# Kernel optimization log

Hardware: AMD Instinct MI355X
Metric: run time of the kernel (lower is better)

The kernel has to match this reference:

```python
import jax, jax.numpy as jnp
import numpy as np

EPS = 1e-5

def _layernorm(x, w, b):
    mu = jnp.mean(x, axis=-1, keepdims=True)
    var = jnp.mean(jnp.square(x - mu), axis=-1, keepdims=True)
    return (x - mu) * jax.lax.rsqrt(var + EPS) * w + b

def setup_inputs() -> dict:
    key = jax.random.key(0)
    ks = jax.random.split(key, 8)
    B, N, C, D = 32, 1024, 4096, 64
    x = jax.random.normal(ks[0], (B, N, C), dtype=jnp.float32)
    gumbel = jax.random.gumbel(ks[1], (B, N, 2), dtype=jnp.float32)
    ln_w = jnp.ones((C,), jnp.float32)
    ln_b = jnp.zeros((C,), jnp.float32)
    w1 = jax.random.normal(ks[2], (C, D), dtype=jnp.float32) * 0.02
    b1 = jnp.zeros((D,), jnp.float32)
    w2 = jax.random.normal(ks[3], (D, 2), dtype=jnp.float32) * 0.02
    b2 = jnp.zeros((2,), jnp.float32)
    return {"x": x, "gumbel": gumbel, "ln_w": ln_w, "ln_b": ln_b,
            "w1": w1, "b1": b1, "w2": w2, "b2": b2}

def reference(x, gumbel, ln_w, ln_b, w1, b1, w2, b2):
    B, N, C = x.shape
    xn = _layernorm(x, ln_w, ln_b)
    local_x = xn[:, :, : C // 2]                      # [B, N, C/2]
    # policy is all-ones -> weighted mean over tokens
    global_x = jnp.mean(xn[:, :, C // 2:], axis=1, keepdims=True)  # [B, 1, C/2]
    feat = jnp.concatenate(
        [local_x, jnp.broadcast_to(global_x, local_x.shape)], axis=-1)  # [B, N, C]
    h = jax.nn.gelu(feat @ w1 + b1, approximate=False)  # [B, N, 64]
    logits = h @ w2 + b2                                # [B, N, 2]
    pred_score = jax.nn.log_softmax(logits, axis=-1)
    # gumbel-softmax (tau=1, hard=True) with straight-through estimator
    y_soft = jax.nn.softmax(pred_score + gumbel, axis=-1)
    hard = jax.nn.one_hot(jnp.argmax(y_soft, axis=-1), 2, dtype=y_soft.dtype)
    y = hard - jax.lax.stop_gradient(y_soft) + y_soft
    keep = y[:, :, 0]                                   # [B, N]
    # dense equivalent of masked_select/split: zero out dropped tokens
    return x * keep[:, :, None]
```

## Files before the change

### kernel.cpp

```cpp
#include <hip/hip_runtime.h>
#include <math.h>

#define B_   32
#define N_   1024
#define C_   4096
#define HC_  2048
#define D_   64
#define NT_  32768
#define BKC_ 32
#define NCH_ (HC_ / BKC_)
#define AST_ 68

__device__ __forceinline__ float4 ld4(const float* p) {
    return *reinterpret_cast<const float4*>(p);
}

__global__ __launch_bounds__(256) void mk1(
        const float* __restrict__ x, const float* __restrict__ lnw,
        const float* __restrict__ lnb, const float* __restrict__ w1,
        float* __restrict__ Pp, float* __restrict__ muv,
        float* __restrict__ rsv, float* __restrict__ part) {
    __shared__ float smem[8704];
    __shared__ float sLow[64], qLow[64];

    float* As0 = smem;
    float* As1 = smem + 2176;
    float* Bs0 = smem + 4352;
    float* Bs1 = smem + 6400;

    const int t = threadIdx.x;
    const int tid = blockIdx.x;
    const int T0 = tid * 64;
    const int rt = t & 15;
    const int dt = t >> 4;
    const int row = t >> 2;
    const int fq = t & 3;
    const int lane = t & 63, w = t >> 6;

    float acc[16];
#pragma unroll
    for (int i = 0; i < 16; ++i) acc[i] = 0.f;
    float sR = 0.f, qR = 0.f;

    float4 xv1, xv2, wv1, wv2;
    float lw1, lw2;
    {
        const float* rp = x + (size_t)(T0 + row) * C_;
        xv1 = ld4(rp + fq * 4);
        xv2 = ld4(rp + 16 + fq * 4);
        const float4* s4 = reinterpret_cast<const float4*>(w1);
        wv1 = s4[t]; wv2 = s4[256 + t];
        lw1 = lnw[t >> 4];
        lw2 = lnw[16 + (t >> 4)];
    }

#pragma unroll 1
    for (int c = 0; c < NCH_; ++c) {
        float* Ab = (c & 1) ? As1 : As0;
        float* Bb = (c & 1) ? Bs1 : Bs0;
        {
            const int kb1 = fq * 4, kb2 = 16 + fq * 4;
            Ab[(kb1 + 0) * AST_ + row] = xv1.x;
            Ab[(kb1 + 1) * AST_ + row] = xv1.y;
            Ab[(kb1 + 2) * AST_ + row] = xv1.z;
            Ab[(kb1 + 3) * AST_ + row] = xv1.w;
            Ab[(kb2 + 0) * AST_ + row] = xv2.x;
            Ab[(kb2 + 1) * AST_ + row] = xv2.y;
            Ab[(kb2 + 2) * AST_ + row] = xv2.z;
            Ab[(kb2 + 3) * AST_ + row] = xv2.w;
            sR += ((xv1.x + xv1.y) + (xv1.z + xv1.w))
                + ((xv2.x + xv2.y) + (xv2.z + xv2.w));
            qR = fmaf(xv1.x, xv1.x, fmaf(xv1.y, xv1.y,
                 fmaf(xv1.z, xv1.z, fmaf(xv1.w, xv1.w, qR))));
            qR = fmaf(xv2.x, xv2.x, fmaf(xv2.y, xv2.y,
                 fmaf(xv2.z, xv2.z, fmaf(xv2.w, xv2.w, qR))));
        }
        {
            float4 v1 = wv1, v2 = wv2;
            v1.x *= lw1; v1.y *= lw1; v1.z *= lw1; v1.w *= lw1;
            v2.x *= lw2; v2.y *= lw2; v2.z *= lw2; v2.w *= lw2;
            float4* b4 = reinterpret_cast<float4*>(Bb);
            b4[t] = v1;
            b4[256 + t] = v2;
        }
        __syncthreads();
        if (c + 1 < NCH_) {
            const int k1 = (c + 1) * BKC_;
            const float* rp = x + (size_t)(T0 + row) * C_ + k1;
            xv1 = ld4(rp + fq * 4);
            xv2 = ld4(rp + 16 + fq * 4);
            const float4* s4 = reinterpret_cast<const float4*>(
                w1 + (size_t)k1 * D_);
            wv1 = s4[t]; wv2 = s4[256 + t];
            lw1 = lnw[k1 + (t >> 4)];
            lw2 = lnw[k1 + 16 + (t >> 4)];
        }
#pragma unroll
        for (int k = 0; k < BKC_; ++k) {
            const float4 a4 = *reinterpret_cast<const float4*>(
                Ab + k * AST_ + rt * 4);
            const float4 b4 = *reinterpret_cast<const float4*>(
                Bb + k * 64 + dt * 4);
            const float av[4] = {a4.x, a4.y, a4.z, a4.w};
            const float bv[4] = {b4.x, b4.y, b4.z, b4.w};
#pragma unroll
            for (int ri = 0; ri < 4; ++ri)
#pragma unroll
                for (int cj = 0; cj < 4; ++cj)
                    acc[ri * 4 + cj] =
                        fmaf(av[ri], bv[cj], acc[ri * 4 + cj]);
        }
    }
#pragma unroll
    for (int ri = 0; ri < 4; ++ri) {
        float* dst = Pp + (size_t)(T0 + rt * 4 + ri) * D_ + dt * 4;
        *reinterpret_cast<float4*>(dst) = make_float4(
            acc[ri * 4 + 0], acc[ri * 4 + 1],
            acc[ri * 4 + 2], acc[ri * 4 + 3]);
    }
    sR += __shfl_xor(sR, 1); qR += __shfl_xor(qR, 1);
    sR += __shfl_xor(sR, 2); qR += __shfl_xor(qR, 2);
    if (fq == 0) { sLow[row] = sR; qLow[row] = qR; }
    __syncthreads();

    float4 wv[8], bv[8], gacc[8];
#pragma unroll
    for (int m = 0; m < 8; ++m) {
        wv[m] = ld4(lnw + HC_ + (m * 64 + lane) * 4);
        bv[m] = ld4(lnb + HC_ + (m * 64 + lane) * 4);
        gacc[m] = make_float4(0.f, 0.f, 0.f, 0.f);
    }
    for (int i = 0; i < 16; ++i) {
        const int r = w * 16 + i;
        const int tok = T0 + r;
        const float* rowp = x + (size_t)tok * C_ + HC_;
        float4 v[8];
        float s = 0.f, q = 0.f;
#pragma unroll
        for (int m = 0; m < 8; ++m) {
            v[m] = ld4(rowp + (m * 64 + lane) * 4);
            s += (v[m].x + v[m].y) + (v[m].z + v[m].w);
            q = fmaf(v[m].x, v[m].x, fmaf(v[m].y, v[m].y,
                fmaf(v[m].z, v[m].z, fmaf(v[m].w, v[m].w, q))));
        }
#pragma unroll
        for (int o = 1; o < 64; o <<= 1) {
            s += __shfl_xor(s, o);
            q += __shfl_xor(q, o);
        }
        const float S = s + sLow[r];
        const float Q = q + qLow[r];
        const float mu = S * (1.f / C_);
        const float rs = rsqrtf(Q * (1.f / C_) - mu * mu + 1e-5f);
        if (lane == 0) {
            muv[tok] = mu;
            rsv[tok] = rs;
        }
#pragma unroll
        for (int m = 0; m < 8; ++m) {
            gacc[m].x += (v[m].x - mu) * rs * wv[m].x + bv[m].x;
            gacc[m].y += (v[m].y - mu) * rs * wv[m].y + bv[m].y;
            gacc[m].z += (v[m].z - mu) * rs * wv[m].z + bv[m].z;
            gacc[m].w += (v[m].w - mu) * rs * wv[m].w + bv[m].w;
        }
    }
    float (*sh)[HC_] = reinterpret_cast<float(*)[HC_]>(smem);
#pragma unroll
    for (int m = 0; m < 8; ++m)
        *reinterpret_cast<float4*>(&sh[w][(m * 64 + lane) * 4]) = gacc[m];
    __syncthreads();
    float* pp = part + (size_t)tid * HC_;
#pragma unroll
    for (int m = 0; m < 8; ++m) {
        const int j = (m * 64 + lane) * 4;
        const float4 a0 = ld4(&sh[0][j]);
        const float4 a1 = ld4(&sh[1][j]);
        const float4 a2 = ld4(&sh[2][j]);
        const float4 a3 = ld4(&sh[3][j]);
        float4 r;
        r.x = (a0.x + a1.x) + (a2.x + a3.x);
        r.y = (a0.y + a1.y) + (a2.y + a3.y);
        r.z = (a0.z + a1.z) + (a2.z + a3.z);
        r.w = (a0.w + a1.w) + (a2.w + a3.w);
        if (w == (m & 3))
            *reinterpret_cast<float4*>(pp + j) = r;
    }
}

__global__ __launch_bounds__(256) void k2a_part(
        const float* __restrict__ part, const float* __restrict__ w1,
        const float* __restrict__ lnw, const float* __restrict__ lnb,
        float* __restrict__ gpart, float* __restrict__ Wpart,
        float* __restrict__ Bpart) {
    __shared__ float Gs[256];
    __shared__ float red[512];
    const int t = threadIdx.x;
    const int d = t & 63, s = t >> 6;
    const int blk = blockIdx.x;
    if (blk < 256) {
        const int b = blk >> 3, jq = blk & 7;
        const int j = jq * 256 + t;
        float a = 0.f;
        for (int k = 0; k < 16; ++k)
            a += part[(size_t)(b * 16 + k) * HC_ + j];
        Gs[t] = a;
        __syncthreads();
        float acc = 0.f;
        const int j0 = jq * 256 + s * 64;
        for (int jj = 0; jj < 64; ++jj)
            acc = fmaf(Gs[s * 64 + jj],
                       w1[(size_t)(HC_ + j0 + jj) * D_ + d], acc);
        red[s * 64 + d] = acc;
        __syncthreads();
        if (s == 0)
            gpart[(size_t)blk * 64 + d] =
                red[d] + red[64 + d] + red[128 + d] + red[192 + d];
    } else {
        const int wq = blk - 256;
        const int c0 = wq * 256 + s * 64;
        float a = 0.f, c2 = 0.f;
        for (int c = c0; c < c0 + 64; ++c) {
            const float wvv = w1[(size_t)c * D_ + d];
            a = fmaf(lnw[c], wvv, a);
            c2 = fmaf(lnb[c], wvv, c2);
        }
        red[s * 64 + d] = a;
        red[256 + s * 64 + d] = c2;
        __syncthreads();
        if (s == 0) {
            Wpart[wq * 64 + d] =
                red[d] + red[64 + d] + red[128 + d] + red[192 + d];
            Bpart[wq * 64 + d] = red[256 + d] + red[320 + d]
                               + red[384 + d] + red[448 + d];
        }
    }
}

__global__ __launch_bounds__(256) void k45_decide_mask(
        const float* __restrict__ Pp, const float* __restrict__ muv,
        const float* __restrict__ rsv, const float* __restrict__ gpart,
        const float* __restrict__ Wpart, const float* __restrict__ Bpart,
        const float* __restrict__ b1, const float* __restrict__ w2,
        const float* __restrict__ b2, const float* __restrict__ gum,
        const float* __restrict__ x, float* __restrict__ out) {
    const int t = threadIdx.x;
    const int lane = t & 63, w = t >> 6;
    const int token = blockIdx.x * 4 + w;
    const int b = token >> 10;

    float W1 = 0.f, Bsv = 0.f, gt = 0.f;
#pragma unroll
    for (int q = 0; q < 8; ++q) {
        W1 += Wpart[q * 64 + lane];
        Bsv += Bpart[q * 64 + lane];
        gt += gpart[(size_t)(b * 8 + q) * 64 + lane];
    }
    gt *= (1.f / N_);

    const float2 gv = *reinterpret_cast<const float2*>(gum + token * 2);
    const float p = Pp[(size_t)token * D_ + lane];
    const float mu = muv[token], rs = rsv[token];
    float h = rs * (p - mu * W1) + Bsv + gt + b1[lane];
    h = 0.5f * h * (1.f + erff(h * 0.70710678118654752f));
    const float2 w2v = *reinterpret_cast<const float2*>(w2 + lane * 2);
    float l0 = h * w2v.x;
    float l1 = h * w2v.y;
#pragma unroll
    for (int o = 1; o < 64; o <<= 1) {
        l0 += __shfl_xor(l0, o);
        l1 += __shfl_xor(l1, o);
    }
    const float z0 = l0 + b2[0] + gv.x;
    const float z1 = l1 + b2[1] + gv.y;

    float4* dst = reinterpret_cast<float4*>(out + (size_t)token * C_);
    if (z0 >= z1) {
        const float4* src =
            reinterpret_cast<const float4*>(x + (size_t)token * C_);
#pragma unroll
        for (int c = 0; c < 16; ++c)
            dst[c * 64 + lane] = src[c * 64 + lane];
    } else {
        const float4 z = make_float4(0.f, 0.f, 0.f, 0.f);
#pragma unroll
        for (int c = 0; c < 16; ++c)
            dst[c * 64 + lane] = z;
    }
}

extern "C" void kernel_launch(void* const* d_in, const int* in_sizes, int n_in,
                              void* d_out, int out_size, void* d_ws,
                              size_t ws_size, hipStream_t stream) {
    const float* x   = (const float*)d_in[0];
    const float* gum = (const float*)d_in[1];
    const float* lnw = (const float*)d_in[2];
    const float* lnb = (const float*)d_in[3];
    const float* w1  = (const float*)d_in[4];
    const float* b1  = (const float*)d_in[5];
    const float* w2  = (const float*)d_in[6];
    const float* b2  = (const float*)d_in[7];
    float* out = (float*)d_out;

    float* wsf   = (float*)d_ws;
    float* Pp    = wsf;
    float* muv   = Pp + (size_t)NT_ * D_;
    float* rsv   = muv + NT_;
    float* part  = rsv + NT_;
    float* gpart = part + (size_t)512 * HC_;
    float* Wpart = gpart + 256 * 64;
    float* Bpart = Wpart + 8 * 64;

    mk1<<<512, 256, 0, stream>>>(x, lnw, lnb, w1, Pp, muv, rsv, part);
    k2a_part<<<264, 256, 0, stream>>>(part, w1, lnw, lnb,
                                      gpart, Wpart, Bpart);
    k45_decide_mask<<<NT_ / 4, 256, 0, stream>>>(Pp, muv, rsv, gpart,
                                                 Wpart, Bpart, b1, w2, b2,
                                                 gum, x, out);
}
```

Baseline: 370.8 us.

## Use split-bf16 MFMA for local projection with fp32 cleanup for near-tie tokens

Replaces the fp32 FMA tile GEMM in the first kernel with bf16 MFMA using a hi/lo split of both activations and pre-scaled weights (three MFMAs per tile) to approximate fp32 accuracy. A prep kernel packs lnw*w1 into bf16 hi/lo fragments. Tokens whose logit margin falls within a small tolerance are recomputed in fp32 by a new cleanup kernel, which rewrites their output row if the keep decision flips. This adds two launches and some extra traffic in exchange for moving the main GEMM onto matrix cores.

```diff
diff --git a/kernel.cpp b/kernel.cpp
--- a/kernel.cpp
+++ b/kernel.cpp
@@ -9,115 +9,137 @@
 #define NT_  32768
 #define BKC_ 32
 #define NCH_ (HC_ / BKC_)
-#define AST_ 68
+#define TAU_ 0.01f
+
+typedef __attribute__((ext_vector_type(8))) short s16x8;
+typedef __attribute__((ext_vector_type(4))) float f32x4;
 
 __device__ __forceinline__ float4 ld4(const float* p) {
     return *reinterpret_cast<const float4*>(p);
 }
-
-__global__ __launch_bounds__(256) void mk1(
+__device__ __forceinline__ unsigned short f2bf(float f) {
+    unsigned int u = __float_as_uint(f);
+    u += 0x7fffu + ((u >> 16) & 1u);
+    return (unsigned short)(u >> 16);
+}
+__device__ __forceinline__ float bf2f(unsigned short s) {
+    return __uint_as_float(((unsigned int)s) << 16);
+}
+
+__global__ __launch_bounds__(64) void k0_prep(
+        const float* __restrict__ lnw, const float* __restrict__ w1,
+        short* __restrict__ whG, short* __restrict__ wlG) {
+    const int lane = threadIdx.x;
+    const int c = blockIdx.x >> 2, ct = blockIdx.x & 3;
+    s16x8 hv, lv;
+#pragma unroll
+    for (int j = 0; j < 8; ++j) {
+        const int k = c * 32 + (lane >> 4) * 8 + j;
+        const int col = ct * 16 + (lane & 15);
+        const float v = lnw[k] * w1[(size_t)k * D_ + col];
+        const unsigned short h = f2bf(v);
+        hv[j] = (short)h;
+        lv[j] = (short)f2bf(v - bf2f(h));
+    }
+    const size_t base = ((size_t)(c * 4 + ct) * 64 + lane) * 8;
+    *reinterpret_cast<s16x8*>(whG + base) = hv;
+    *reinterpret_cast<s16x8*>(wlG + base) = lv;
+}
+
+__global__ __launch_bounds__(256) void mk1m(
         const float* __restrict__ x, const float* __restrict__ lnw,
-        const float* __restrict__ lnb, const float* __restrict__ w1,
-        float* __restrict__ Pp, float* __restrict__ muv,
-        float* __restrict__ rsv, float* __restrict__ part) {
-    __shared__ float smem[8704];
+        const float* __restrict__ lnb, const short* __restrict__ whG,
+        const short* __restrict__ wlG, float* __restrict__ Pp,
+        float* __restrict__ muv, float* __restrict__ rsv,
+        float* __restrict__ part) {
+    __shared__ float smem[8192];
     __shared__ float sLow[64], qLow[64];
-
-    float* As0 = smem;
-    float* As1 = smem + 2176;
-    float* Bs0 = smem + 4352;
-    float* Bs1 = smem + 6400;
+    short* S = reinterpret_cast<short*>(smem);
 
     const int t = threadIdx.x;
     const int tid = blockIdx.x;
     const int T0 = tid * 64;
-    const int rt = t & 15;
-    const int dt = t >> 4;
-    const int row = t >> 2;
-    const int fq = t & 3;
+    const int row = t >> 2, fq = t & 3;
     const int lane = t & 63, w = t >> 6;
 
-    float acc[16];
-#pragma unroll
-    for (int i = 0; i < 16; ++i) acc[i] = 0.f;
+    f32x4 acc[4];
+#pragma unroll
+    for (int ct = 0; ct < 4; ++ct)
+#pragma unroll
+        for (int r = 0; r < 4; ++r) acc[ct][r] = 0.f;
     float sR = 0.f, qR = 0.f;
 
-    float4 xv1, xv2, wv1, wv2;
-    float lw1, lw2;
+    float4 xv1, xv2;
+    s16x8 bh[4], bl[4], bh2[4], bl2[4];
     {
         const float* rp = x + (size_t)(T0 + row) * C_;
-        xv1 = ld4(rp + fq * 4);
-        xv2 = ld4(rp + 16 + fq * 4);
-        const float4* s4 = reinterpret_cast<const float4*>(w1);
-        wv1 = s4[t]; wv2 = s4[256 + t];
-        lw1 = lnw[t >> 4];
-        lw2 = lnw[16 + (t >> 4)];
+        xv1 = ld4(rp + fq * 8);
+        xv2 = ld4(rp + fq * 8 + 4);
+        const s16x8* wp = reinterpret_cast<const s16x8*>(whG);
+        const s16x8* lp = reinterpret_cast<const s16x8*>(wlG);
+#pragma unroll
+        for (int ct = 0; ct < 4; ++ct) {
+            bh[ct] = wp[(size_t)ct * 64 + lane];
+            bl[ct] = lp[(size_t)ct * 64 + lane];
+        }
     }
 
 #pragma unroll 1
     for (int c = 0; c < NCH_; ++c) {
-        float* Ab = (c & 1) ? As1 : As0;
-        float* Bb = (c & 1) ? Bs1 : Bs0;
+        short* H = S + (c & 1) * 4096;
+        short* L = H + 2048;
         {
-            const int kb1 = fq * 4, kb2 = 16 + fq * 4;
-            Ab[(kb1 + 0) * AST_ + row] = xv1.x;
-            Ab[(kb1 + 1) * AST_ + row] = xv1.y;
-            Ab[(kb1 + 2) * AST_ + row] = xv1.z;
-            Ab[(kb1 + 3) * AST_ + row] = xv1.w;
-            Ab[(kb2 + 0) * AST_ + row] = xv2.x;
-            Ab[(kb2 + 1) * AST_ + row] = xv2.y;
-            Ab[(kb2 + 2) * AST_ + row] = xv2.z;
-            Ab[(kb2 + 3) * AST_ + row] = xv2.w;
-            sR += ((xv1.x + xv1.y) + (xv1.z + xv1.w))
-                + ((xv2.x + xv2.y) + (xv2.z + xv2.w));
-            qR = fmaf(xv1.x, xv1.x, fmaf(xv1.y, xv1.y,
-                 fmaf(xv1.z, xv1.z, fmaf(xv1.w, xv1.w, qR))));
-            qR = fmaf(xv2.x, xv2.x, fmaf(xv2.y, xv2.y,
-                 fmaf(xv2.z, xv2.z, fmaf(xv2.w, xv2.w, qR))));
-        }
-        {
-            float4 v1 = wv1, v2 = wv2;
-            v1.x *= lw1; v1.y *= lw1; v1.z *= lw1; v1.w *= lw1;
-            v2.x *= lw2; v2.y *= lw2; v2.z *= lw2; v2.w *= lw2;
-            float4* b4 = reinterpret_cast<float4*>(Bb);
-            b4[t] = v1;
-            b4[256 + t] = v2;
+            const int slot = (row >> 4) * 64 + fq * 16 + (row & 15);
+            const float xs[8] = {xv1.x, xv1.y, xv1.z, xv1.w,
+                                 xv2.x, xv2.y, xv2.z, xv2.w};
+            s16x8 hv, lv;
+#pragma unroll
+            for (int j = 0; j < 8; ++j) {
+                const unsigned short h = f2bf(xs[j]);
+                hv[j] = (short)h;
+                lv[j] = (short)f2bf(xs[j] - bf2f(h));
+            }
+            *reinterpret_cast<s16x8*>(H + slot * 8) = hv;
+            *reinterpret_cast<s16x8*>(L + slot * 8) = lv;
+            sR += ((xs[0] + xs[1]) + (xs[2] + xs[3]))
+                + ((xs[4] + xs[5]) + (xs[6] + xs[7]));
+#pragma unroll
+            for (int j = 0; j < 8; ++j) qR = fmaf(xs[j], xs[j], qR);
         }
         __syncthreads();
         if (c + 1 < NCH_) {
-            const int k1 = (c + 1) * BKC_;
-            const float* rp = x + (size_t)(T0 + row) * C_ + k1;
-            xv1 = ld4(rp + fq * 4);
-            xv2 = ld4(rp + 16 + fq * 4);
-            const float4* s4 = reinterpret_cast<const float4*>(
-                w1 + (size_t)k1 * D_);
-            wv1 = s4[t]; wv2 = s4[256 + t];
-            lw1 = lnw[k1 + (t >> 4)];
-            lw2 = lnw[k1 + 16 + (t >> 4)];
-        }
-#pragma unroll
-        for (int k = 0; k < BKC_; ++k) {
-            const float4 a4 = *reinterpret_cast<const float4*>(
-                Ab + k * AST_ + rt * 4);
-            const float4 b4 = *reinterpret_cast<const float4*>(
-                Bb + k * 64 + dt * 4);
-            const float av[4] = {a4.x, a4.y, a4.z, a4.w};
-            const float bv[4] = {b4.x, b4.y, b4.z, b4.w};
-#pragma unroll
-            for (int ri = 0; ri < 4; ++ri)
-#pragma unroll
-                for (int cj = 0; cj < 4; ++cj)
-                    acc[ri * 4 + cj] =
-                        fmaf(av[ri], bv[cj], acc[ri * 4 + cj]);
-        }
-    }
-#pragma unroll
-    for (int ri = 0; ri < 4; ++ri) {
-        float* dst = Pp + (size_t)(T0 + rt * 4 + ri) * D_ + dt * 4;
-        *reinterpret_cast<float4*>(dst) = make_float4(
-            acc[ri * 4 + 0], acc[ri * 4 + 1],
-            acc[ri * 4 + 2], acc[ri * 4 + 3]);
-    }
+            const float* rp = x + (size_t)(T0 + row) * C_ + (c + 1) * BKC_;
+            xv1 = ld4(rp + fq * 8);
+            xv2 = ld4(rp + fq * 8 + 4);
+            const s16x8* wp = reinterpret_cast<const s16x8*>(whG);
+            const s16x8* lp = reinterpret_cast<const s16x8*>(wlG);
+#pragma unroll
+            for (int ct = 0; ct < 4; ++ct) {
+                bh2[ct] = wp[((size_t)(c + 1) * 4 + ct) * 64 + lane];
+                bl2[ct] = lp[((size_t)(c + 1) * 4 + ct) * 64 + lane];
+            }
+        }
+        const s16x8 Ah = *reinterpret_cast<const s16x8*>(H + (w * 64 + lane) * 8);
+        const s16x8 Al = *reinterpret_cast<const s16x8*>(L + (w * 64 + lane) * 8);
+#pragma unroll
+        for (int ct = 0; ct < 4; ++ct) {
+            acc[ct] = __builtin_amdgcn_mfma_f32_16x16x32_bf16(
+                Ah, bh[ct], acc[ct], 0, 0, 0);
+            acc[ct] = __builtin_amdgcn_mfma_f32_16x16x32_bf16(
+                Al, bh[ct], acc[ct], 0, 0, 0);
+            acc[ct] = __builtin_amdgcn_mfma_f32_16x16x32_bf16(
+                Ah, bl[ct], acc[ct], 0, 0, 0);
+        }
+#pragma unroll
+        for (int ct = 0; ct < 4; ++ct) { bh[ct] = bh2[ct]; bl[ct] = bl2[ct]; }
+    }
+#pragma unroll
+    for (int ct = 0; ct < 4; ++ct)
+#pragma unroll
+        for (int r = 0; r < 4; ++r) {
+            const int tok = T0 + w * 16 + (lane >> 4) * 4 + r;
+            Pp[(size_t)tok * D_ + ct * 16 + (lane & 15)] = acc[ct][r];
+        }
     sR += __shfl_xor(sR, 1); qR += __shfl_xor(qR, 1);
     sR += __shfl_xor(sR, 2); qR += __shfl_xor(qR, 2);
     if (fq == 0) { sLow[row] = sR; qLow[row] = qR; }
@@ -242,7 +264,8 @@
         const float* __restrict__ Wpart, const float* __restrict__ Bpart,
         const float* __restrict__ b1, const float* __restrict__ w2,
         const float* __restrict__ b2, const float* __restrict__ gum,
-        const float* __restrict__ x, float* __restrict__ out) {
+        const float* __restrict__ x, float* __restrict__ out,
+        float* __restrict__ dzv) {
     const int t = threadIdx.x;
     const int lane = t & 63, w = t >> 6;
     const int token = blockIdx.x * 4 + w;
@@ -272,11 +295,79 @@
     }
     const float z0 = l0 + b2[0] + gv.x;
     const float z1 = l1 + b2[1] + gv.y;
+    if (lane == 0) dzv[token] = z0 - z1;
 
     float4* dst = reinterpret_cast<float4*>(out + (size_t)token * C_);
     if (z0 >= z1) {
         const float4* src =
             reinterpret_cast<const float4*>(x + (size_t)token * C_);
+#pragma unroll
+        for (int c = 0; c < 16; ++c)
+            dst[c * 64 + lane] = src[c * 64 + lane];
+    } else {
+        const float4 z = make_float4(0.f, 0.f, 0.f, 0.f);
+#pragma unroll
+        for (int c = 0; c < 16; ++c)
+            dst[c * 64 + lane] = z;
+    }
+}
+
+__global__ __launch_bounds__(256) void k6_cleanup(
+        const float* __restrict__ x, const float* __restrict__ lnw,
+        const float* __restrict__ w1, const float* __restrict__ muv,
+        const float* __restrict__ rsv, const float* __restrict__ gpart,
+        const float* __restrict__ Wpart, const float* __restrict__ Bpart,
+        const float* __restrict__ b1, const float* __restrict__ w2,
+        const float* __restrict__ b2, const float* __restrict__ gum,
+        const float* __restrict__ dzv, float* __restrict__ out) {
+    const int t = threadIdx.x;
+    const int lane = t & 63, w = t >> 6;
+    const int token = blockIdx.x * 4 + w;
+    const float dz = dzv[token];
+    if (fabsf(dz) >= TAU_) return;
+
+    const float* xr = x + (size_t)token * C_;
+    float p0 = 0.f, p1 = 0.f, p2 = 0.f, p3 = 0.f;
+    for (int k = 0; k < HC_; k += 4) {
+        const float4 xk = ld4(xr + k);
+        const float4 wk = ld4(lnw + k);
+        p0 = fmaf(xk.x * wk.x, w1[(size_t)(k + 0) * D_ + lane], p0);
+        p1 = fmaf(xk.y * wk.y, w1[(size_t)(k + 1) * D_ + lane], p1);
+        p2 = fmaf(xk.z * wk.z, w1[(size_t)(k + 2) * D_ + lane], p2);
+        p3 = fmaf(xk.w * wk.w, w1[(size_t)(k + 3) * D_ + lane], p3);
+    }
+    const float p = (p0 + p1) + (p2 + p3);
+
+    const int b = token >> 10;
+    float W1 = 0.f, Bsv = 0.f, gt = 0.f;
+#pragma unroll
+    for (int q = 0; q < 8; ++q) {
+        W1 += Wpart[q * 64 + lane];
+        Bsv += Bpart[q * 64 + lane];
+        gt += gpart[(size_t)(b * 8 + q) * 64 + lane];
+    }
+    gt *= (1.f / N_);
+    const float2 gv = *reinterpret_cast<const float2*>(gum + token * 2);
+    const float mu = muv[token], rs = rsv[token];
+    float h = rs * (p - mu * W1) + Bsv + gt + b1[lane];
+    h = 0.5f * h * (1.f + erff(h * 0.70710678118654752f));
+    const float2 w2v = *reinterpret_cast<const float2*>(w2 + lane * 2);
+    float l0 = h * w2v.x;
+    float l1 = h * w2v.y;
+#pragma unroll
+    for (int o = 1; o < 64; o <<= 1) {
+        l0 += __shfl_xor(l0, o);
+        l1 += __shfl_xor(l1, o);
+    }
+    const float z0 = l0 + b2[0] + gv.x;
+    const float z1 = l1 + b2[1] + gv.y;
+    const bool keepNew = (z0 >= z1);
+    const bool keepOld = (dz >= 0.f);
+    if (keepNew == keepOld) return;
+
+    float4* dst = reinterpret_cast<float4*>(out + (size_t)token * C_);
+    if (keepNew) {
+        const float4* src = reinterpret_cast<const float4*>(xr);
 #pragma unroll
         for (int c = 0; c < 16; ++c)
             dst[c * 64 + lane] = src[c * 64 + lane];
@@ -309,11 +400,18 @@
     float* gpart = part + (size_t)512 * HC_;
     float* Wpart = gpart + 256 * 64;
     float* Bpart = Wpart + 8 * 64;
-
-    mk1<<<512, 256, 0, stream>>>(x, lnw, lnb, w1, Pp, muv, rsv, part);
+    float* dzv   = Bpart + 8 * 64;
+    short* whG   = (short*)(dzv + NT_);
+    short* wlG   = whG + (size_t)131072;
+
+    k0_prep<<<256, 64, 0, stream>>>(lnw, w1, whG, wlG);
+    mk1m<<<512, 256, 0, stream>>>(x, lnw, lnb, whG, wlG, Pp, muv, rsv, part);
     k2a_part<<<264, 256, 0, stream>>>(part, w1, lnw, lnb,
                                       gpart, Wpart, Bpart);
     k45_decide_mask<<<NT_ / 4, 256, 0, stream>>>(Pp, muv, rsv, gpart,
                                                  Wpart, Bpart, b1, w2, b2,
-                                                 gum, x, out);
-}
+                                                 gum, x, out, dzv);
+    k6_cleanup<<<NT_ / 4, 256, 0, stream>>>(x, lnw, w1, muv, rsv, gpart,
+                                            Wpart, Bpart, b1, w2, b2,
+                                            gum, dzv, out);
+}
```

Result: slower. 428.6 us (+15.6%).
